# Kernel tuning notes

Measured on AMD Instinct MI355X. Metric: run time of the kernel, lower is better.

The kernel has to match this reference:

```python
import jax, jax.numpy as jnp
import numpy as np

B, REPR, FEAT, HID = 4096, 39200, 256, 1024
GATE, MHID, E, K, SDIM, ADIM = 256, 256, 32, 4, 24, 7

def _lin(key, fin, fout):
    kw, kb = jax.random.split(key)
    w = jax.random.normal(kw, (fin, fout), jnp.float32) / np.sqrt(fin)
    b = jax.random.normal(kb, (fout,), jnp.float32) * 0.01
    return w, b

def setup_inputs() -> dict:
    key = jax.random.key(0)
    ks = jax.random.split(key, 16)
    obs = jax.random.normal(ks[0], (B, REPR), jnp.float32)
    obs_sensor = jax.random.normal(ks[1], (B, SDIM), jnp.float32)
    std = jnp.ones((1,), jnp.float32)
    trunk_w, trunk_b = _lin(ks[2], REPR, FEAT)
    ln_g = jnp.ones((FEAT,), jnp.float32); ln_b = jnp.zeros((FEAT,), jnp.float32)
    se1_w, se1_b = _lin(ks[3], SDIM, HID)
    se2_w, se2_b = _lin(ks[4], HID, FEAT)
    fu1_w, fu1_b = _lin(ks[5], FEAT, HID)
    fu2_w, fu2_b = _lin(ks[6], HID, FEAT)
    p1_w, p1_b = _lin(ks[7], FEAT, HID)
    g1_w, g1_b = _lin(ks[8], HID, GATE)
    g2_w, g2_b = _lin(ks[9], GATE, E)
    e1_w = jax.random.normal(ks[10], (E, HID, MHID), jnp.float32) / np.sqrt(HID)
    e1_b = jnp.zeros((E, MHID), jnp.float32)
    e2_w = jax.random.normal(ks[11], (E, MHID, HID), jnp.float32) / np.sqrt(MHID)
    e2_b = jnp.zeros((E, HID), jnp.float32)
    p2_w, p2_b = _lin(ks[12], HID, ADIM)
    return dict(obs=obs, std=std, obs_sensor=obs_sensor, trunk_w=trunk_w, trunk_b=trunk_b,
                ln_g=ln_g, ln_b=ln_b, se1_w=se1_w, se1_b=se1_b, se2_w=se2_w, se2_b=se2_b,
                fu1_w=fu1_w, fu1_b=fu1_b, fu2_w=fu2_w, fu2_b=fu2_b, p1_w=p1_w, p1_b=p1_b,
                g1_w=g1_w, g1_b=g1_b, g2_w=g2_w, g2_b=g2_b, e1_w=e1_w, e1_b=e1_b,
                e2_w=e2_w, e2_b=e2_b, p2_w=p2_w, p2_b=p2_b)

def _layernorm(x, g, b, eps=1e-5):
    mu = jnp.mean(x, -1, keepdims=True)
    var = jnp.var(x, -1, keepdims=True)
    return (x - mu) * jax.lax.rsqrt(var + eps) * g + b

def reference(obs, std, obs_sensor, trunk_w, trunk_b, ln_g, ln_b, se1_w, se1_b, se2_w, se2_b,
              fu1_w, fu1_b, fu2_w, fu2_b, p1_w, p1_b, g1_w, g1_b, g2_w, g2_b,
              e1_w, e1_b, e2_w, e2_b, p2_w, p2_b):
    # trunk: Linear -> LayerNorm -> Tanh
    h = jnp.tanh(_layernorm(obs @ trunk_w + trunk_b, ln_g, ln_b))
    # StateEncoder: h + MLP(state), then fusion MLP
    s = jax.nn.relu(obs_sensor @ se1_w + se1_b) @ se2_w + se2_b
    h = h + s
    h = jax.nn.relu(h @ fu1_w + fu1_b) @ fu2_w + fu2_b
    # policy1
    x = jax.nn.relu(h @ p1_w + p1_b)
    # MoE: gate MLP -> top-4 of 32 experts, softmax over top-k, weighted combine
    logits = jax.nn.relu(x @ g1_w + g1_b) @ g2_w + g2_b          # [B, E]
    topv, topi = jax.lax.top_k(logits, K)                         # [B, K]
    topw = jax.nn.softmax(topv, axis=-1)                          # renormalized
    comb = jnp.zeros(logits.shape, logits.dtype).at[jnp.arange(logits.shape[0])[:, None], topi].set(topw)  # [B, E]
    h1 = jax.nn.relu(jnp.einsum('bi,eih->beh', x, e1_w) + e1_b[None])  # [B, E, MHID]
    y = jnp.einsum('beh,eho->beo', h1, e2_w) + e2_b[None]              # [B, E, HID]
    x_moe = jnp.einsum('be,beo->bo', comb, y)                          # [B, HID]
    # load-balancing aux loss (Switch-style)
    probs = jax.nn.softmax(logits, axis=-1)
    importance = jnp.mean(probs, axis=0)                               # [E]
    load = jnp.mean((comb > 0).astype(logits.dtype), axis=0)           # [E]
    aux_loss = logits.shape[-1] * jnp.sum(importance * load)
    # policy2: ReLU -> Linear, then tanh -> mean of TruncatedNormal
    mu = jnp.tanh(jax.nn.relu(x_moe) @ p2_w + p2_b)
    return mu, aux_loss
```

## Files before the change

kernel.cpp:

```cpp
#include <hip/hip_runtime.h>
#include <stdint.h>

typedef _Float16 half_t;
typedef half_t half2v __attribute__((ext_vector_type(2)));
typedef half_t half8  __attribute__((ext_vector_type(8)));
typedef float  f32x4v __attribute__((ext_vector_type(4)));

typedef __attribute__((address_space(1))) void as1_void;
typedef __attribute__((address_space(3))) void as3_void;
#define GLOAD_LDS16(gp, lp) \
  __builtin_amdgcn_global_load_lds((as1_void*)(gp), (as3_void*)(lp), 16, 0, 0)

constexpr int MAXTILES = 288;
constexpr int SLOTCAP  = MAXTILES * 64;
constexpr float LO_SCALE = 2048.f;
constexpr float LO_INV   = 1.f / 2048.f;

constexpr size_t PLANE_TRUNK = (size_t)256 * 39200;
constexpr size_t PLANE_SMALL = (size_t)262144;
constexpr size_t OFF_WT_TRUNK = 0;
constexpr size_t OFF_WT_SE2 = OFF_WT_TRUNK + PLANE_TRUNK * 2 * 2;
constexpr size_t OFF_WT_FU1 = OFF_WT_SE2 + PLANE_SMALL * 2 * 2;
constexpr size_t OFF_WT_FU2 = OFF_WT_FU1 + PLANE_SMALL * 2 * 2;
constexpr size_t OFF_WT_P1  = OFF_WT_FU2 + PLANE_SMALL * 2 * 2;
constexpr size_t OFF_WT_G1  = OFF_WT_P1  + PLANE_SMALL * 2 * 2;
constexpr size_t OFF_WT_E1  = OFF_WT_G1  + PLANE_SMALL * 2 * 2;
constexpr size_t OFF_WT_E2  = OFF_WT_E1  + (size_t)32 * 262144 * 2;
constexpr size_t OFF_PART   = OFF_WT_E2  + (size_t)32 * 262144 * 2;
constexpr size_t SZ_PART    = (size_t)12 * 4096 * 256 * 4;
constexpr size_t OFF_YBUF   = OFF_PART;
constexpr size_t OFF_S1     = OFF_PART + SZ_PART;
constexpr size_t OFF_H1     = OFF_S1;
constexpr size_t OFF_SOUT   = OFF_S1   + (size_t)4096 * 1024 * 4;
constexpr size_t OFF_HBUF   = OFF_SOUT + (size_t)4096 * 256 * 4;
constexpr size_t OFF_H2     = OFF_HBUF + (size_t)4096 * 256 * 4;
constexpr size_t OFF_XBUF   = OFF_H2   + (size_t)4096 * 256 * 4;
constexpr size_t OFF_GBUF   = OFF_XBUF + (size_t)4096 * 1024 * 4;
constexpr size_t OFF_LOGITS = OFF_GBUF + (size_t)4096 * 256 * 4;
constexpr size_t OFF_RTI    = OFF_LOGITS + (size_t)4096 * 32 * 4;
constexpr size_t OFF_RTW    = OFF_RTI  + (size_t)4096 * 4 * 4;
constexpr size_t OFF_CTRL   = OFF_RTW  + (size_t)4096 * 4 * 4;
constexpr size_t SZ_CTRL    = 4096;
constexpr size_t OFF_SLOTB  = OFF_CTRL + SZ_CTRL;
constexpr size_t OFF_R2S    = OFF_SLOTB + (size_t)SLOTCAP * 4;
constexpr size_t OFF_H1E    = OFF_R2S  + (size_t)4096 * 4 * 4;

__global__ __launch_bounds__(256) void cvt_k(
    const float* __restrict__ trunk_w, const float* __restrict__ se2_w,
    const float* __restrict__ fu1_w,  const float* __restrict__ fu2_w,
    const float* __restrict__ p1_w,   const float* __restrict__ g1_w,
    const float* __restrict__ e1_w,   const float* __restrict__ e2_w,
    char* __restrict__ ws)
{
    __shared__ float t[32][33];
    int id = blockIdx.x;
    const float* src; half_t* dh; int N, Kp, kt, nt; size_t plane;
    if (id < 9800)       { src = trunk_w; dh = (half_t*)(ws + OFF_WT_TRUNK); plane = PLANE_TRUNK; N=256;  Kp=39200; kt=id>>3; nt=id&7; }
    else if (id < 10056) { int r=id-9800;  src = se2_w; dh=(half_t*)(ws+OFF_WT_SE2); plane=PLANE_SMALL; N=256;  Kp=1024; kt=r>>3; nt=r&7; }
    else if (id < 10312) { int r=id-10056; src = fu1_w; dh=(half_t*)(ws+OFF_WT_FU1); plane=PLANE_SMALL; N=1024; Kp=256;  kt=r>>5; nt=r&31; }
    else if (id < 10568) { int r=id-10312; src = fu2_w; dh=(half_t*)(ws+OFF_WT_FU2); plane=PLANE_SMALL; N=256;  Kp=1024; kt=r>>3; nt=r&7; }
    else if (id < 10824) { int r=id-10568; src = p1_w;  dh=(half_t*)(ws+OFF_WT_P1);  plane=PLANE_SMALL; N=1024; Kp=256;  kt=r>>5; nt=r&31; }
    else if (id < 11080) { int r=id-10824; src = g1_w;  dh=(half_t*)(ws+OFF_WT_G1);  plane=PLANE_SMALL; N=256;  Kp=1024; kt=r>>3; nt=r&7; }
    else if (id < 19272) { int r=id-11080; int e=r>>8; int rr=r&255;
        src = e1_w + (size_t)e*262144; dh = (half_t*)(ws+OFF_WT_E1) + (size_t)e*262144;
        plane = 0; N=256; Kp=1024; kt=rr>>3; nt=rr&7; }
    else                 { int r=id-19272; int e=r>>8; int rr=r&255;
        src = e2_w + (size_t)e*262144; dh = (half_t*)(ws+OFF_WT_E2) + (size_t)e*262144;
        plane = 0; N=1024; Kp=256; kt=rr>>5; nt=rr&31; }

    int k0 = kt * 32, n0 = nt * 32;
    int tx = threadIdx.x & 31, ty = threadIdx.x >> 5;
#pragma unroll
    for (int i = 0; i < 4; ++i) {
        int r = i * 8 + ty;
        t[tx][r] = src[(size_t)(k0 + r) * N + (n0 + tx)];
    }
    __syncthreads();
#pragma unroll
    for (int i = 0; i < 4; ++i) {
        int rn = i * 8 + ty;
        float v = t[rn][tx];
        size_t di = (size_t)(n0 + rn) * Kp + (k0 + tx);
        half_t hv = (half_t)v;
        dh[di] = hv;
        if (plane) dh[di + plane] = (half_t)((v - (float)hv) * LO_SCALE);
    }
}

template<int ACT, int PARTIAL>
__global__ __launch_bounds__(256) void gemm_prec(
    const float* __restrict__ A, const half_t* __restrict__ Wt,
    const float* __restrict__ bias, void* __restrict__ Outp,
    int KpA, int KpW, int ksteps, int NoutStride, size_t planeB)
{
    __shared__ __attribute__((aligned(16))) char lds[(64 + 64 + 256 + 256) * 64];
    char* ldsAh = lds;
    char* ldsAl = lds + 4096;
    char* ldsBh = lds + 8192;
    char* ldsBl = lds + 8192 + 16384;
    const int tid = threadIdx.x;
    const int lane = tid & 63, wid = tid >> 6;
    const int mrow = lane & 15, quad = lane >> 4;

    const int m0 = blockIdx.x * 64;
    int n0, ks0, ks1;
    if (PARTIAL) {
        n0 = 0;
        int S = gridDim.y;
        ks0 = (int)(((long)blockIdx.y * ksteps) / S);
        ks1 = (int)(((long)(blockIdx.y + 1) * ksteps) / S);
    } else { n0 = blockIdx.y * 256; ks0 = 0; ks1 = ksteps; }

    const int ar = tid >> 2, ap = tid & 3;
    const int ac = ap ^ ((ar >> 1) & 3);
    const float* a32 = A + (size_t)(m0 + ar) * KpA + ac * 8;

    const half_t* bsrcH[4];
    int bdst[4];
#pragma unroll
    for (int j = 0; j < 4; ++j) {
        int lin = j * 256 + tid;
        int br = lin >> 2, bp = lin & 3;
        int bc = bp ^ ((br >> 1) & 3);
        bsrcH[j] = Wt + (size_t)(n0 + br) * KpW + bc * 8;
        bdst[j] = lin * 16;
    }

    int aoff[4], boff[4];
#pragma unroll
    for (int mt = 0; mt < 4; ++mt) {
        int r = mt * 16 + mrow;
        aoff[mt] = r * 64 + ((quad ^ ((r >> 1) & 3)) << 4);
    }
#pragma unroll
    for (int nt = 0; nt < 4; ++nt) {
        int r = wid * 64 + nt * 16 + mrow;
        boff[nt] = r * 64 + ((quad ^ ((r >> 1) & 3)) << 4);
    }

    f32x4v zero4 = {0.f, 0.f, 0.f, 0.f};
    f32x4v accM[4][4], accC[4][4];
#pragma unroll
    for (int mt = 0; mt < 4; ++mt)
#pragma unroll
        for (int nt = 0; nt < 4; ++nt) { accM[mt][nt] = zero4; accC[mt][nt] = zero4; }

    f32x4v pf0 = *(const f32x4v*)(a32 + ks0 * 32);
    f32x4v pf1 = *(const f32x4v*)(a32 + ks0 * 32 + 4);

    for (int ks = ks0; ks < ks1; ++ks) {
        const int kk = ks * 32;
        half8 ah, al;
#pragma unroll
        for (int u = 0; u < 4; ++u) {
            float v0 = pf0[u], v1 = pf1[u];
            half_t h0 = (half_t)v0, h1 = (half_t)v1;
            ah[u] = h0; ah[4 + u] = h1;
            al[u]     = (half_t)((v0 - (float)h0) * LO_SCALE);
            al[4 + u] = (half_t)((v1 - (float)h1) * LO_SCALE);
        }
        *(half8*)(ldsAh + tid * 16) = ah;
        *(half8*)(ldsAl + tid * 16) = al;
#pragma unroll
        for (int j = 0; j < 4; ++j) {
            GLOAD_LDS16(bsrcH[j] + kk, ldsBh + bdst[j]);
            GLOAD_LDS16(bsrcH[j] + planeB + kk, ldsBl + bdst[j]);
        }
        __syncthreads();
        if (ks + 1 < ks1) {
            pf0 = *(const f32x4v*)(a32 + (ks + 1) * 32);
            pf1 = *(const f32x4v*)(a32 + (ks + 1) * 32 + 4);
        }
        half8 fah[4], fal[4], fbh[4], fbl[4];
#pragma unroll
        for (int mt = 0; mt < 4; ++mt) {
            fah[mt] = *(const half8*)(ldsAh + aoff[mt]);
            fal[mt] = *(const half8*)(ldsAl + aoff[mt]);
        }
#pragma unroll
        for (int nt = 0; nt < 4; ++nt) {
            fbh[nt] = *(const half8*)(ldsBh + boff[nt]);
            fbl[nt] = *(const half8*)(ldsBl + boff[nt]);
        }
#pragma unroll
        for (int mt = 0; mt < 4; ++mt)
#pragma unroll
            for (int nt = 0; nt < 4; ++nt) {
                accM[mt][nt] = __builtin_amdgcn_mfma_f32_16x16x32_f16(fah[mt], fbh[nt], accM[mt][nt], 0, 0, 0);
                accC[mt][nt] = __builtin_amdgcn_mfma_f32_16x16x32_f16(fal[mt], fbh[nt], accC[mt][nt], 0, 0, 0);
                accC[mt][nt] = __builtin_amdgcn_mfma_f32_16x16x32_f16(fah[mt], fbl[nt], accC[mt][nt], 0, 0, 0);
            }
        __syncthreads();
    }

    if (PARTIAL) {
        float* po = (float*)Outp + (size_t)blockIdx.y * 4096 * 256;
#pragma unroll
        for (int mt = 0; mt < 4; ++mt)
#pragma unroll
            for (int nt = 0; nt < 4; ++nt) {
                int col = wid * 64 + nt * 16 + mrow;
#pragma unroll
                for (int r = 0; r < 4; ++r) {
                    int row = m0 + mt * 16 + quad * 4 + r;
                    po[(size_t)row * 256 + col] = accM[mt][nt][r] + accC[mt][nt][r] * LO_INV;
                }
            }
    } else {
        float* fo = (float*)Outp;
#pragma unroll
        for (int nt = 0; nt < 4; ++nt) {
            int col = n0 + wid * 64 + nt * 16 + mrow;
            float bv = bias[col];
#pragma unroll
            for (int mt = 0; mt < 4; ++mt)
#pragma unroll
                for (int r = 0; r < 4; ++r) {
                    int row = m0 + mt * 16 + quad * 4 + r;
                    float v = accM[mt][nt][r] + accC[mt][nt][r] * LO_INV + bv;
                    if (ACT == 1) v = fmaxf(v, 0.f);
                    fo[(size_t)row * NoutStride + col] = v;
                }
        }
    }
}

template<int AF32, int MODE, int ACT>
__global__ __launch_bounds__(256) void gemm_fast(
    const void* __restrict__ Aptr, const half_t* __restrict__ Wt0,
    const float* __restrict__ bias0, half_t* __restrict__ Outp,
    int KpA, int KpW, int ksteps, int NoutStride,
    const int* __restrict__ slotb, const int* __restrict__ t2e,
    const int* __restrict__ ntp, int wtStride, int biasStride)
{
    __shared__ __attribute__((aligned(16))) char lds[(64 + 256) * 64];
    char* ldsA = lds;
    char* ldsB = lds + 64 * 64;
    const int tid = threadIdx.x;
    const int lane = tid & 63, wid = tid >> 6;
    const int mrow = lane & 15, quad = lane >> 4;

    if ((int)blockIdx.x >= *ntp) return;
    int e = t2e[blockIdx.x];
    const int m0 = blockIdx.x * 64;
    const int n0 = (MODE == 2) ? blockIdx.y * 256 : 0;
    const half_t* wt = Wt0 + (size_t)e * wtStride;
    const float* bias = bias0 + (size_t)e * biasStride;

    const int ar = tid >> 2, ap = tid & 3;
    const int ac = ap ^ ((ar >> 1) & 3);
    long arow;
    if (MODE == 1) { int b = slotb[m0 + ar]; arow = (b < 0) ? 0 : b; }
    else arow = m0 + ar;
    const float*  a32 = (const float*)Aptr  + (size_t)arow * KpA + ac * 8;
    const half_t* a16 = (const half_t*)Aptr + (size_t)arow * KpA + ac * 8;

    const half_t* bsrc[4];
    int bdst[4];
#pragma unroll
    for (int j = 0; j < 4; ++j) {
        int lin = j * 256 + tid;
        int br = lin >> 2, bp = lin & 3;
        int bc = bp ^ ((br >> 1) & 3);
        bsrc[j] = wt + (size_t)(n0 + br) * KpW + bc * 8;
        bdst[j] = lin * 16;
    }

    int aoff[4], boff[4];
#pragma unroll
    for (int mt = 0; mt < 4; ++mt) {
        int r = mt * 16 + mrow;
        aoff[mt] = r * 64 + ((quad ^ ((r >> 1) & 3)) << 4);
    }
#pragma unroll
    for (int nt = 0; nt < 4; ++nt) {
        int r = wid * 64 + nt * 16 + mrow;
        boff[nt] = r * 64 + ((quad ^ ((r >> 1) & 3)) << 4);
    }

    f32x4v zero4 = {0.f, 0.f, 0.f, 0.f};
    f32x4v acc[4][4];
#pragma unroll
    for (int mt = 0; mt < 4; ++mt)
#pragma unroll
        for (int nt = 0; nt < 4; ++nt) acc[mt][nt] = zero4;

    f32x4v pf0 = zero4, pf1 = zero4;
    if (AF32) { pf0 = *(const f32x4v*)(a32); pf1 = *(const f32x4v*)(a32 + 4); }

    for (int ks = 0; ks < ksteps; ++ks) {
        const int kk = ks * 32;
        if (AF32) {
            half8 av;
#pragma unroll
            for (int u = 0; u < 4; ++u) { av[u] = (half_t)pf0[u]; av[4 + u] = (half_t)pf1[u]; }
            *(half8*)(ldsA + tid * 16) = av;
        } else {
            GLOAD_LDS16(a16 + kk, ldsA + tid * 16);
        }
#pragma unroll
        for (int j = 0; j < 4; ++j) GLOAD_LDS16(bsrc[j] + kk, ldsB + bdst[j]);
        __syncthreads();
        if (AF32 && ks + 1 < ksteps) {
            pf0 = *(const f32x4v*)(a32 + (ks + 1) * 32);
            pf1 = *(const f32x4v*)(a32 + (ks + 1) * 32 + 4);
        }
        half8 afr[4], bfr[4];
#pragma unroll
        for (int mt = 0; mt < 4; ++mt) afr[mt] = *(const half8*)(ldsA + aoff[mt]);
#pragma unroll
        for (int nt = 0; nt < 4; ++nt) bfr[nt] = *(const half8*)(ldsB + boff[nt]);
#pragma unroll
        for (int mt = 0; mt < 4; ++mt)
#pragma unroll
            for (int nt = 0; nt < 4; ++nt)
                acc[mt][nt] = __builtin_amdgcn_mfma_f32_16x16x32_f16(afr[mt], bfr[nt], acc[mt][nt], 0, 0, 0);
        __syncthreads();
    }

#pragma unroll
    for (int nt = 0; nt < 4; ++nt) {
        int col = n0 + wid * 64 + nt * 16 + mrow;
        float bv = bias[col];
#pragma unroll
        for (int mt = 0; mt < 4; ++mt)
#pragma unroll
            for (int r = 0; r < 4; ++r) {
                int row = m0 + mt * 16 + quad * 4 + r;
                float v = acc[mt][nt][r] + bv;
                if (ACT == 1) v = fmaxf(v, 0.f);
                Outp[(size_t)row * NoutStride + col] = (half_t)v;
            }
    }
}

template<int ACT>
__global__ __launch_bounds__(256) void reduce4_k(const float* __restrict__ part,
    const float* __restrict__ bias, float* __restrict__ outp)
{
    size_t i = ((size_t)blockIdx.x * 256 + threadIdx.x) * 4;
    f32x4v v = *(const f32x4v*)(part + i);
    v += *(const f32x4v*)(part + (size_t)1 * 4096 * 256 + i);
    v += *(const f32x4v*)(part + (size_t)2 * 4096 * 256 + i);
    v += *(const f32x4v*)(part + (size_t)3 * 4096 * 256 + i);
    int col = (int)(i & 255);
    v += *(const f32x4v*)(bias + col);
    if (ACT) {
#pragma unroll
        for (int u = 0; u < 4; ++u) v[u] = fmaxf(v[u], 0.f);
    }
    *(f32x4v*)(outp + i) = v;
}

__global__ __launch_bounds__(256) void se1_k(const float* __restrict__ os,
    const float* __restrict__ w, const float* __restrict__ b, float* __restrict__ out)
{
    __shared__ float lo[4][24];
    int r0 = blockIdx.x * 4;
    int t = threadIdx.x;
    if (t < 96) { int r = t / 24, k = t % 24; lo[r][k] = os[(size_t)(r0 + r) * 24 + k]; }
    __syncthreads();
    int c0 = t * 4;
    f32x4v acc[4];
    f32x4v bv = *(const f32x4v*)(b + c0);
#pragma unroll
    for (int r = 0; r < 4; ++r) acc[r] = bv;
    for (int k = 0; k < 24; ++k) {
        f32x4v wv = *(const f32x4v*)(w + (size_t)k * 1024 + c0);
#pragma unroll
        for (int r = 0; r < 4; ++r) acc[r] += lo[r][k] * wv;
    }
#pragma unroll
    for (int r = 0; r < 4; ++r) {
#pragma unroll
        for (int u = 0; u < 4; ++u) acc[r][u] = fmaxf(acc[r][u], 0.f);
        *(f32x4v*)(out + (size_t)(r0 + r) * 1024 + c0) = acc[r];
    }
}

__global__ __launch_bounds__(256) void lnfuse_k(const float* __restrict__ part,
    const float* __restrict__ tb, const float* __restrict__ lng, const float* __restrict__ lnb,
    const float* __restrict__ sout, float* __restrict__ hbuf)
{
    int row = blockIdx.x, col = threadIdx.x;
    size_t idx = (size_t)row * 256 + col;
    float t = tb[col];
#pragma unroll
    for (int s = 0; s < 12; ++s) t += part[(size_t)s * 4096 * 256 + idx];
    float s1 = t, s2 = t * t;
#pragma unroll
    for (int o = 32; o >= 1; o >>= 1) { s1 += __shfl_xor(s1, o, 64); s2 += __shfl_xor(s2, o, 64); }
    __shared__ float rs1[4], rs2[4];
    int wid = threadIdx.x >> 6;
    if ((threadIdx.x & 63) == 0) { rs1[wid] = s1; rs2[wid] = s2; }
    __syncthreads();
    float S1 = rs1[0] + rs1[1] + rs1[2] + rs1[3];
    float S2 = rs2[0] + rs2[1] + rs2[2] + rs2[3];
    float mu = S1 * (1.f / 256.f);
    float var = S2 * (1.f / 256.f) - mu * mu;
    float h0 = tanhf((t - mu) * rsqrtf(var + 1e-5f) * lng[col] + lnb[col]);
    hbuf[idx] = h0 + sout[idx];
}

__global__ __launch_bounds__(256) void logits_k(const float* __restrict__ g,
    const float* __restrict__ w, const float* __restrict__ bb, float* __restrict__ out)
{
    __shared__ float lw[256 * 32];
    __shared__ __attribute__((aligned(16))) float lg[8 * 256];
    int tid = threadIdx.x;
    for (int i = tid; i < 8192; i += 256) lw[i] = w[i];
    size_t base = (size_t)blockIdx.x * 8 * 256;
    *(f32x4v*)(lg + tid * 8)     = *(const f32x4v*)(g + base + tid * 8);
    *(f32x4v*)(lg + tid * 8 + 4) = *(const f32x4v*)(g + base + tid * 8 + 4);
    __syncthreads();
    int r = tid >> 5, c = tid & 31;
    const float* gr = lg + r * 256;
    float acc = bb[c];
    for (int k = 0; k < 256; k += 4) {
        acc += gr[k]   * lw[(k)   * 32 + c];
        acc += gr[k+1] * lw[(k+1) * 32 + c];
        acc += gr[k+2] * lw[(k+2) * 32 + c];
        acc += gr[k+3] * lw[(k+3) * 32 + c];
    }
    out[(size_t)blockIdx.x * 256 + tid] = acc;
}

__global__ __launch_bounds__(256) void topk_k(const float* __restrict__ logits,
    int* __restrict__ rti, float* __restrict__ rtw, float* __restrict__ imp, int* __restrict__ cnt)
{
    __shared__ float simp[32];
    __shared__ int scnt[32];
    int tid = threadIdx.x;
    if (tid < 32) { simp[tid] = 0.f; scnt[tid] = 0; }
    __syncthreads();
    int b = blockIdx.x * 256 + tid;
    const float* row = logits + (size_t)b * 32;
    float v0 = -1e30f, v1 = -1e30f, v2 = -1e30f, v3 = -1e30f;
    int i0 = 0, i1 = 0, i2 = 0, i3 = 0;
    for (int i = 0; i < 32; ++i) {
        float x = row[i];
        if (x > v0)      { v3=v2;i3=i2; v2=v1;i2=i1; v1=v0;i1=i0; v0=x;i0=i; }
        else if (x > v1) { v3=v2;i3=i2; v2=v1;i2=i1; v1=x;i1=i; }
        else if (x > v2) { v3=v2;i3=i2; v2=x;i2=i; }
        else if (x > v3) { v3=x;i3=i; }
    }
    float e1 = expf(v1 - v0), e2 = expf(v2 - v0), e3 = expf(v3 - v0);
    float inv = 1.f / (1.f + e1 + e2 + e3);
    rti[b*4+0] = i0; rti[b*4+1] = i1; rti[b*4+2] = i2; rti[b*4+3] = i3;
    rtw[b*4+0] = inv; rtw[b*4+1] = e1*inv; rtw[b*4+2] = e2*inv; rtw[b*4+3] = e3*inv;
    atomicAdd(&scnt[i0], 1); atomicAdd(&scnt[i1], 1);
    atomicAdd(&scnt[i2], 1); atomicAdd(&scnt[i3], 1);
    float dsum = 0.f;
    for (int i = 0; i < 32; ++i) dsum += expf(row[i] - v0);
    float dinv = 1.f / dsum;
    for (int i = 0; i < 32; ++i) {
        float p = expf(row[i] - v0) * dinv;
#pragma unroll
        for (int o = 32; o >= 1; o >>= 1) p += __shfl_xor(p, o, 64);
        if ((tid & 63) == 0) atomicAdd(&simp[i], p);
    }
    __syncthreads();
    if (tid < 32) { atomicAdd(&imp[tid], simp[tid]); atomicAdd(&cnt[tid], scnt[tid]); }
}

__global__ void prefix_k(const int* __restrict__ cnt, int* __restrict__ poff,
                         int* __restrict__ ntp, int* __restrict__ t2e)
{
    if (threadIdx.x == 0) {
        int acc = 0;
        for (int e = 0; e < 32; ++e) {
            poff[e] = acc * 64;
            int pt = (cnt[e] + 63) >> 6;
            for (int t = 0; t < pt; ++t) t2e[acc + t] = e;
            acc += pt;
        }
        poff[32] = acc * 64;
        *ntp = acc;
    }
}

__global__ __launch_bounds__(256) void scatter_k(const int* __restrict__ rti,
    int* __restrict__ cnt2, const int* __restrict__ poff,
    int* __restrict__ slotb, int* __restrict__ r2s)
{
    int b = blockIdx.x * 256 + threadIdx.x;
#pragma unroll
    for (int j = 0; j < 4; ++j) {
        int e = rti[b * 4 + j];
        int p = atomicAdd(&cnt2[e], 1);
        int s = poff[e] + p;
        slotb[s] = b;
        r2s[b * 4 + j] = s;
    }
}

__global__ __launch_bounds__(256) void comb_p2_k(const half_t* __restrict__ ybuf,
    const int* __restrict__ r2s, const float* __restrict__ rtw,
    const float* __restrict__ p2w, const float* __restrict__ p2b, float* __restrict__ outp)
{
    __shared__ float lw[7 * 1024];
    int tid = threadIdx.x;
    for (int i = tid; i < 7168; i += 256) {
        int c = i >> 10, k = i & 1023;
        lw[i] = p2w[(size_t)k * 7 + c];
    }
    __syncthreads();
    int wid = tid >> 6, lane = tid & 63;
    int b = blockIdx.x * 4 + wid;
    int s0 = r2s[b*4+0], s1_ = r2s[b*4+1], s2_ = r2s[b*4+2], s3_ = r2s[b*4+3];
    float w0 = rtw[b*4+0], w1 = rtw[b*4+1], w2 = rtw[b*4+2], w3 = rtw[b*4+3];
    float xm[16];
#pragma unroll
    for (int u = 0; u < 8; ++u) {
        int k = u * 128 + lane * 2;
        half2v y0 = *(const half2v*)(ybuf + (size_t)s0  * 1024 + k);
        half2v y1 = *(const half2v*)(ybuf + (size_t)s1_ * 1024 + k);
        half2v y2 = *(const half2v*)(ybuf + (size_t)s2_ * 1024 + k);
        half2v y3 = *(const half2v*)(ybuf + (size_t)s3_ * 1024 + k);
        float a  = w0*(float)y0[0] + w1*(float)y1[0] + w2*(float)y2[0] + w3*(float)y3[0];
        float bq = w0*(float)y0[1] + w1*(float)y1[1] + w2*(float)y2[1] + w3*(float)y3[1];
        xm[u*2]   = fmaxf(a, 0.f);
        xm[u*2+1] = fmaxf(bq, 0.f);
    }
    float p[7] = {0, 0, 0, 0, 0, 0, 0};
#pragma unroll
    for (int u = 0; u < 8; ++u) {
        int k = u * 128 + lane * 2;
#pragma unroll
        for (int c = 0; c < 7; ++c)
            p[c] += xm[u*2] * lw[c * 1024 + k] + xm[u*2+1] * lw[c * 1024 + k + 1];
    }
#pragma unroll
    for (int c = 0; c < 7; ++c) {
#pragma unroll
        for (int o = 32; o >= 1; o >>= 1) p[c] += __shfl_xor(p[c], o, 64);
    }
    if (lane == 0) {
#pragma unroll
        for (int c = 0; c < 7; ++c) outp[(size_t)b * 7 + c] = tanhf(p[c] + p2b[c]);
    }
}

__global__ void aux_k(const float* __restrict__ imp, const int* __restrict__ cnt,
                      float* __restrict__ outp)
{
    int t = threadIdx.x;
    float v = (t < 32) ? imp[t] * (float)cnt[t] : 0.f;
#pragma unroll
    for (int o = 32; o >= 1; o >>= 1) v += __shfl_xor(v, o, 64);
    if (t == 0) outp[0] = 32.f * v / (4096.f * 4096.f);
}

extern "C" void kernel_launch(void* const* d_in, const int* in_sizes, int n_in,
                              void* d_out, int out_size, void* d_ws, size_t ws_size,
                              hipStream_t stream)
{
    (void)in_sizes; (void)n_in; (void)out_size; (void)ws_size;
    const float* obs        = (const float*)d_in[0];
    const float* obs_sensor = (const float*)d_in[2];
    const float* trunk_w    = (const float*)d_in[3];
    const float* trunk_b    = (const float*)d_in[4];
    const float* ln_g       = (const float*)d_in[5];
    const float* ln_b       = (const float*)d_in[6];
    const float* se1_w      = (const float*)d_in[7];
    const float* se1_b      = (const float*)d_in[8];
    const float* se2_b      = (const float*)d_in[10];
    const float* fu1_b      = (const float*)d_in[12];
    const float* fu2_b      = (const float*)d_in[14];
    const float* p1_b       = (const float*)d_in[16];
    const float* g1_b       = (const float*)d_in[18];
    const float* g2_w       = (const float*)d_in[19];
    const float* g2_b       = (const float*)d_in[20];
    const float* e1_b       = (const float*)d_in[22];
    const float* e2_b       = (const float*)d_in[24];
    const float* p2_w       = (const float*)d_in[25];
    const float* p2_b       = (const float*)d_in[26];

    char* ws = (char*)d_ws;
    half_t* WT_TRUNK = (half_t*)(ws + OFF_WT_TRUNK);
    half_t* WT_SE2   = (half_t*)(ws + OFF_WT_SE2);
    half_t* WT_FU1   = (half_t*)(ws + OFF_WT_FU1);
    half_t* WT_FU2   = (half_t*)(ws + OFF_WT_FU2);
    half_t* WT_P1    = (half_t*)(ws + OFF_WT_P1);
    half_t* WT_G1    = (half_t*)(ws + OFF_WT_G1);
    half_t* WT_E1    = (half_t*)(ws + OFF_WT_E1);
    half_t* WT_E2    = (half_t*)(ws + OFF_WT_E2);
    float*  PART     = (float*)(ws + OFF_PART);
    half_t* YBUF     = (half_t*)(ws + OFF_YBUF);
    float*  S1buf    = (float*)(ws + OFF_S1);
    float*  H1buf    = (float*)(ws + OFF_H1);
    float*  SOUT     = (float*)(ws + OFF_SOUT);
    float*  HBUF     = (float*)(ws + OFF_HBUF);
    float*  H2buf    = (float*)(ws + OFF_H2);
    float*  XBUF     = (float*)(ws + OFF_XBUF);
    float*  GBUF     = (float*)(ws + OFF_GBUF);
    float*  LOGITS   = (float*)(ws + OFF_LOGITS);
    int*    RTI      = (int*)(ws + OFF_RTI);
    float*  RTW      = (float*)(ws + OFF_RTW);
    float*  IMP      = (float*)(ws + OFF_CTRL);
    int*    CNT      = (int*)(ws + OFF_CTRL + 128);
    int*    CNT2     = (int*)(ws + OFF_CTRL + 256);
    int*    POFF     = (int*)(ws + OFF_CTRL + 384);
    int*    NTP      = (int*)(ws + OFF_CTRL + 520);
    int*    T2E      = (int*)(ws + OFF_CTRL + 524);
    int*    SLOTB    = (int*)(ws + OFF_SLOTB);
    int*    R2S      = (int*)(ws + OFF_R2S);
    half_t* H1E      = (half_t*)(ws + OFF_H1E);

    hipMemsetAsync(ws + OFF_CTRL, 0, SZ_CTRL, stream);
    hipMemsetAsync(ws + OFF_SLOTB, 0xFF, (size_t)SLOTCAP * 4, stream);

    cvt_k<<<27464, 256, 0, stream>>>(trunk_w, (const float*)d_in[9], (const float*)d_in[11],
        (const float*)d_in[13], (const float*)d_in[15], (const float*)d_in[17],
        (const float*)d_in[21], (const float*)d_in[23], ws);

    se1_k<<<1024, 256, 0, stream>>>(obs_sensor, se1_w, se1_b, S1buf);
    gemm_prec<0,1><<<dim3(64,4), 256, 0, stream>>>(S1buf, WT_SE2, nullptr, PART,
        1024, 1024, 32, 256, PLANE_SMALL);
    reduce4_k<0><<<1024, 256, 0, stream>>>(PART, se2_b, SOUT);
    gemm_prec<0,1><<<dim3(64,12), 256, 0, stream>>>(obs, WT_TRUNK, nullptr, PART,
        39200, 39200, 1225, 256, PLANE_TRUNK);
    lnfuse_k<<<4096, 256, 0, stream>>>(PART, trunk_b, ln_g, ln_b, SOUT, HBUF);
    gemm_prec<1,0><<<dim3(64,4), 256, 0, stream>>>(HBUF, WT_FU1, fu1_b, H1buf,
        256, 256, 8, 1024, PLANE_SMALL);
    gemm_prec<0,1><<<dim3(64,4), 256, 0, stream>>>(H1buf, WT_FU2, nullptr, PART,
        1024, 1024, 32, 256, PLANE_SMALL);
    reduce4_k<0><<<1024, 256, 0, stream>>>(PART, fu2_b, H2buf);
    gemm_prec<1,0><<<dim3(64,4), 256, 0, stream>>>(H2buf, WT_P1, p1_b, XBUF,
        256, 256, 8, 1024, PLANE_SMALL);
    gemm_prec<0,1><<<dim3(64,4), 256, 0, stream>>>(XBUF, WT_G1, nullptr, PART,
        1024, 1024, 32, 256, PLANE_SMALL);
    reduce4_k<1><<<1024, 256, 0, stream>>>(PART, g1_b, GBUF);
    logits_k<<<512, 256, 0, stream>>>(GBUF, g2_w, g2_b, LOGITS);
    topk_k<<<16, 256, 0, stream>>>(LOGITS, RTI, RTW, IMP, CNT);
    prefix_k<<<1, 64, 0, stream>>>(CNT, POFF, NTP, T2E);
    scatter_k<<<16, 256, 0, stream>>>(RTI, CNT2, POFF, SLOTB, R2S);
    gemm_fast<1,1,1><<<dim3(MAXTILES,1), 256, 0, stream>>>(XBUF, WT_E1, e1_b, H1E,
        1024, 1024, 32, 256, SLOTB, T2E, NTP, 262144, 256);
    gemm_fast<0,2,0><<<dim3(MAXTILES,4), 256, 0, stream>>>(H1E, WT_E2, e2_b, YBUF,
        256, 256, 8, 1024, nullptr, T2E, NTP, 262144, 1024);
    comb_p2_k<<<1024, 256, 0, stream>>>(YBUF, R2S, RTW, p2_w, p2_b, (float*)d_out);
    aux_k<<<1, 64, 0, stream>>>(IMP, CNT, (float*)d_out + 28672);
}
```

Before: 1.768 ms.

## Double-buffer LDS in GEMM kernels and cut trunk split-K from 12 to 8

Both GEMM kernels now use two LDS buffers. The next K-step's weight tiles (and A tile) are issued into the spare buffer while MFMAs run on the current one, and the per-step sync becomes a manual waitcnt plus barrier instead of two __syncthreads. The trunk GEMM's split-K count drops from 12 to 8, with the LN reduction adjusted to match, which removes partial-sum traffic but gives fewer blocks. gemm_prec's LDS doubles to about 80KB per block, which can reduce occupancy, and the hand-written vmcnt accounting is fragile.

```diff
diff --git a/kernel.cpp b/kernel.cpp
--- a/kernel.cpp
+++ b/kernel.cpp
@@ -93,11 +93,8 @@
     const float* __restrict__ bias, void* __restrict__ Outp,
     int KpA, int KpW, int ksteps, int NoutStride, size_t planeB)
 {
-    __shared__ __attribute__((aligned(16))) char lds[(64 + 64 + 256 + 256) * 64];
-    char* ldsAh = lds;
-    char* ldsAl = lds + 4096;
-    char* ldsBh = lds + 8192;
-    char* ldsBl = lds + 8192 + 16384;
+    constexpr int BUF = (64 + 64 + 256 + 256) * 64;
+    __shared__ __attribute__((aligned(16))) char lds[2 * BUF];
     const int tid = threadIdx.x;
     const int lane = tid & 63, wid = tid >> 6;
     const int mrow = lane & 15, quad = lane >> 4;
@@ -148,8 +145,13 @@
     f32x4v pf0 = *(const f32x4v*)(a32 + ks0 * 32);
     f32x4v pf1 = *(const f32x4v*)(a32 + ks0 * 32 + 4);
 
-    for (int ks = ks0; ks < ks1; ++ks) {
-        const int kk = ks * 32;
+    {
+        const int kk = ks0 * 32;
+#pragma unroll
+        for (int j = 0; j < 4; ++j) {
+            GLOAD_LDS16(bsrcH[j] + kk, lds + 8192 + bdst[j]);
+            GLOAD_LDS16(bsrcH[j] + planeB + kk, lds + 8192 + 16384 + bdst[j]);
+        }
         half8 ah, al;
 #pragma unroll
         for (int u = 0; u < 4; ++u) {
@@ -159,28 +161,51 @@
             al[u]     = (half_t)((v0 - (float)h0) * LO_SCALE);
             al[4 + u] = (half_t)((v1 - (float)h1) * LO_SCALE);
         }
-        *(half8*)(ldsAh + tid * 16) = ah;
-        *(half8*)(ldsAl + tid * 16) = al;
-#pragma unroll
-        for (int j = 0; j < 4; ++j) {
-            GLOAD_LDS16(bsrcH[j] + kk, ldsBh + bdst[j]);
-            GLOAD_LDS16(bsrcH[j] + planeB + kk, ldsBl + bdst[j]);
-        }
-        __syncthreads();
+        *(half8*)(lds + tid * 16) = ah;
+        *(half8*)(lds + 4096 + tid * 16) = al;
+        int kn = (ks0 + 1 < ks1) ? ks0 + 1 : ks0;
+        pf0 = *(const f32x4v*)(a32 + kn * 32);
+        pf1 = *(const f32x4v*)(a32 + kn * 32 + 4);
+    }
+    asm volatile("s_waitcnt vmcnt(2) lgkmcnt(0)" ::: "memory");
+    __builtin_amdgcn_s_barrier();
+
+    int cur = 0;
+    for (int ks = ks0; ks < ks1; ++ks) {
+        char* cb = lds + cur * BUF;
+        char* nb = lds + (cur ^ 1) * BUF;
         if (ks + 1 < ks1) {
-            pf0 = *(const f32x4v*)(a32 + (ks + 1) * 32);
-            pf1 = *(const f32x4v*)(a32 + (ks + 1) * 32 + 4);
+            const int kk = (ks + 1) * 32;
+#pragma unroll
+            for (int j = 0; j < 4; ++j) {
+                GLOAD_LDS16(bsrcH[j] + kk, nb + 8192 + bdst[j]);
+                GLOAD_LDS16(bsrcH[j] + planeB + kk, nb + 8192 + 16384 + bdst[j]);
+            }
+            half8 ah, al;
+#pragma unroll
+            for (int u = 0; u < 4; ++u) {
+                float v0 = pf0[u], v1 = pf1[u];
+                half_t h0 = (half_t)v0, h1 = (half_t)v1;
+                ah[u] = h0; ah[4 + u] = h1;
+                al[u]     = (half_t)((v0 - (float)h0) * LO_SCALE);
+                al[4 + u] = (half_t)((v1 - (float)h1) * LO_SCALE);
+            }
+            *(half8*)(nb + tid * 16) = ah;
+            *(half8*)(nb + 4096 + tid * 16) = al;
+            int kn = (ks + 2 < ks1) ? ks + 2 : ks + 1;
+            pf0 = *(const f32x4v*)(a32 + kn * 32);
+            pf1 = *(const f32x4v*)(a32 + kn * 32 + 4);
         }
         half8 fah[4], fal[4], fbh[4], fbl[4];
 #pragma unroll
         for (int mt = 0; mt < 4; ++mt) {
-            fah[mt] = *(const half8*)(ldsAh + aoff[mt]);
-            fal[mt] = *(const half8*)(ldsAl + aoff[mt]);
+            fah[mt] = *(const half8*)(cb + aoff[mt]);
+            fal[mt] = *(const half8*)(cb + 4096 + aoff[mt]);
         }
 #pragma unroll
         for (int nt = 0; nt < 4; ++nt) {
-            fbh[nt] = *(const half8*)(ldsBh + boff[nt]);
-            fbl[nt] = *(const half8*)(ldsBl + boff[nt]);
+            fbh[nt] = *(const half8*)(cb + 8192 + boff[nt]);
+            fbl[nt] = *(const half8*)(cb + 8192 + 16384 + boff[nt]);
         }
 #pragma unroll
         for (int mt = 0; mt < 4; ++mt)
@@ -190,7 +215,9 @@
                 accC[mt][nt] = __builtin_amdgcn_mfma_f32_16x16x32_f16(fal[mt], fbh[nt], accC[mt][nt], 0, 0, 0);
                 accC[mt][nt] = __builtin_amdgcn_mfma_f32_16x16x32_f16(fah[mt], fbl[nt], accC[mt][nt], 0, 0, 0);
             }
-        __syncthreads();
+        asm volatile("s_waitcnt vmcnt(2) lgkmcnt(0)" ::: "memory");
+        __builtin_amdgcn_s_barrier();
+        cur ^= 1;
     }
 
     if (PARTIAL) {
@@ -233,9 +260,8 @@
     const int* __restrict__ slotb, const int* __restrict__ t2e,
     const int* __restrict__ ntp, int wtStride, int biasStride)
 {
-    __shared__ __attribute__((aligned(16))) char lds[(64 + 256) * 64];
-    char* ldsA = lds;
-    char* ldsB = lds + 64 * 64;
+    constexpr int BUF = (64 + 256) * 64;
+    __shared__ __attribute__((aligned(16))) char lds[2 * BUF];
     const int tid = threadIdx.x;
     const int lane = tid & 63, wid = tid >> 6;
     const int mrow = lane & 15, quad = lane >> 4;
@@ -288,34 +314,57 @@
     f32x4v pf0 = zero4, pf1 = zero4;
     if (AF32) { pf0 = *(const f32x4v*)(a32); pf1 = *(const f32x4v*)(a32 + 4); }
 
-    for (int ks = 0; ks < ksteps; ++ks) {
-        const int kk = ks * 32;
+    {
+        if (!AF32) GLOAD_LDS16(a16, lds + tid * 16);
+#pragma unroll
+        for (int j = 0; j < 4; ++j) GLOAD_LDS16(bsrc[j], lds + 4096 + bdst[j]);
         if (AF32) {
             half8 av;
 #pragma unroll
             for (int u = 0; u < 4; ++u) { av[u] = (half_t)pf0[u]; av[4 + u] = (half_t)pf1[u]; }
-            *(half8*)(ldsA + tid * 16) = av;
-        } else {
-            GLOAD_LDS16(a16 + kk, ldsA + tid * 16);
-        }
-#pragma unroll
-        for (int j = 0; j < 4; ++j) GLOAD_LDS16(bsrc[j] + kk, ldsB + bdst[j]);
-        __syncthreads();
-        if (AF32 && ks + 1 < ksteps) {
-            pf0 = *(const f32x4v*)(a32 + (ks + 1) * 32);
-            pf1 = *(const f32x4v*)(a32 + (ks + 1) * 32 + 4);
+            *(half8*)(lds + tid * 16) = av;
+            int kn = (1 < ksteps) ? 1 : 0;
+            pf0 = *(const f32x4v*)(a32 + kn * 32);
+            pf1 = *(const f32x4v*)(a32 + kn * 32 + 4);
+        }
+    }
+    if (AF32) asm volatile("s_waitcnt vmcnt(2) lgkmcnt(0)" ::: "memory");
+    else      asm volatile("s_waitcnt vmcnt(0) lgkmcnt(0)" ::: "memory");
+    __builtin_amdgcn_s_barrier();
+
+    int cur = 0;
+    for (int ks = 0; ks < ksteps; ++ks) {
+        char* cb = lds + cur * BUF;
+        char* nb = lds + (cur ^ 1) * BUF;
+        if (ks + 1 < ksteps) {
+            const int kk = (ks + 1) * 32;
+            if (!AF32) GLOAD_LDS16(a16 + kk, nb + tid * 16);
+#pragma unroll
+            for (int j = 0; j < 4; ++j) GLOAD_LDS16(bsrc[j] + kk, nb + 4096 + bdst[j]);
+            if (AF32) {
+                half8 av;
+#pragma unroll
+                for (int u = 0; u < 4; ++u) { av[u] = (half_t)pf0[u]; av[4 + u] = (half_t)pf1[u]; }
+                *(half8*)(nb + tid * 16) = av;
+                int kn = (ks + 2 < ksteps) ? ks + 2 : ks + 1;
+                pf0 = *(const f32x4v*)(a32 + kn * 32);
+                pf1 = *(const f32x4v*)(a32 + kn * 32 + 4);
+            }
         }
         half8 afr[4], bfr[4];
 #pragma unroll
-        for (int mt = 0; mt < 4; ++mt) afr[mt] = *(const half8*)(ldsA + aoff[mt]);
-#pragma unroll
-        for (int nt = 0; nt < 4; ++nt) bfr[nt] = *(const half8*)(ldsB + boff[nt]);
+        for (int mt = 0; mt < 4; ++mt) afr[mt] = *(const half8*)(cb + aoff[mt]);
+#pragma unroll
+        for (int nt = 0; nt < 4; ++nt) bfr[nt] = *(const half8*)(cb + 4096 + boff[nt]);
 #pragma unroll
         for (int mt = 0; mt < 4; ++mt)
 #pragma unroll
             for (int nt = 0; nt < 4; ++nt)
                 acc[mt][nt] = __builtin_amdgcn_mfma_f32_16x16x32_f16(afr[mt], bfr[nt], acc[mt][nt], 0, 0, 0);
-        __syncthreads();
+        if (AF32) asm volatile("s_waitcnt vmcnt(2) lgkmcnt(0)" ::: "memory");
+        else      asm volatile("s_waitcnt vmcnt(0) lgkmcnt(0)" ::: "memory");
+        __builtin_amdgcn_s_barrier();
+        cur ^= 1;
     }
 
 #pragma unroll
@@ -386,7 +435,7 @@
     size_t idx = (size_t)row * 256 + col;
     float t = tb[col];
 #pragma unroll
-    for (int s = 0; s < 12; ++s) t += part[(size_t)s * 4096 * 256 + idx];
+    for (int s = 0; s < 8; ++s) t += part[(size_t)s * 4096 * 256 + idx];
     float s1 = t, s2 = t * t;
 #pragma unroll
     for (int o = 32; o >= 1; o >>= 1) { s1 += __shfl_xor(s1, o, 64); s2 += __shfl_xor(s2, o, 64); }
@@ -618,7 +667,7 @@
     gemm_prec<0,1><<<dim3(64,4), 256, 0, stream>>>(S1buf, WT_SE2, nullptr, PART,
         1024, 1024, 32, 256, PLANE_SMALL);
     reduce4_k<0><<<1024, 256, 0, stream>>>(PART, se2_b, SOUT);
-    gemm_prec<0,1><<<dim3(64,12), 256, 0, stream>>>(obs, WT_TRUNK, nullptr, PART,
+    gemm_prec<0,1><<<dim3(64,8), 256, 0, stream>>>(obs, WT_TRUNK, nullptr, PART,
         39200, 39200, 1225, 256, PLANE_TRUNK);
     lnfuse_k<<<4096, 256, 0, stream>>>(PART, trunk_b, ln_g, ln_b, SOUT, HBUF);
     gemm_prec<1,0><<<dim3(64,4), 256, 0, stream>>>(HBUF, WT_FU1, fu1_b, H1buf,
```

Result: faster. 1.632 ms (-7.7%).
